# Performance work log

Measured on AMD Instinct MI355X. Metric: run time of the kernel, lower is better.

## Reference

```python
import jax, jax.numpy as jnp
import numpy as np

PATCH = 7            # args.corr_size (local correlation window)
R = PATCH // 2       # displacement radius


def _disps():
    return [(dy, dx) for dy in range(PATCH) for dx in range(PATCH)]


def setup_inputs() -> dict:
    key = jax.random.key(0)
    k1, k2, k3 = jax.random.split(key, 3)
    B, De, Do, T, H, W = 4, 64, 64, 4, 128, 128
    m_in = jax.random.normal(k1, (B, De, T, H, W), jnp.float32)
    m_out = jax.random.normal(k2, (B, Do, T, H, W), jnp.float32)
    q_in = jax.random.normal(k3, (B, De, H, W), jnp.float32)
    const = jnp.zeros((1,), jnp.float32)  # learnable constant (init 0)
    return {"m_in": m_in, "m_out": m_out, "q_in": q_in, "const": const}


def reference(m_in, m_out, q_in, const):
    B, De, T, H, W = m_in.shape
    Do = m_out.shape[1]
    P2 = PATCH * PATCH
    # --- functionCorrelation over all T frames at once ---
    # p[b, d, t, h, w] = sum_c q[b,c,h,w] * m_in[b,c,t,h+dy-R,w+dx-R]  (zero-padded)
    mp = jnp.pad(m_in, ((0, 0), (0, 0), (0, 0), (R, R), (R, R)))
    p = jnp.stack(
        [jnp.einsum('bchw,bcthw->bthw', q_in, mp[:, :, :, dy:dy + H, dx:dx + W])
         for dy, dx in _disps()],
        axis=1)  # [B, P2, T, H, W]  (matches torch stack(dim=2) then disp at dim=1)
    # --- softmax over stacked (P2*T [+1 const]) channels ---
    logits = p.reshape(B, P2 * T, H, W)
    cst = jnp.broadcast_to(const.reshape(1, 1, 1, 1), (B, 1, H, W))
    logits = jnp.concatenate([logits, cst], axis=1)
    attn = jax.nn.softmax(logits, axis=1)[:, :-1]  # drop constant channel
    attn = attn.reshape(B, P2, T, H, W)
    # --- functionCorrelationTranspose summed over T (attention read) ---
    # mem[b,c,h,w] = sum_{t,d} attn[b,d,t,h,w] * m_out[b,c,t,h+dy-R,w+dx-R]
    vp = jnp.pad(m_out, ((0, 0), (0, 0), (0, 0), (R, R), (R, R)))
    mem = jnp.zeros((B, Do, H, W), m_out.dtype)
    for d, (dy, dx) in enumerate(_disps()):
        mem = mem + jnp.einsum('bthw,bcthw->bchw', attn[:, d], vp[:, :, :, dy:dy + H, dx:dx + W])
    return mem, attn
```

## Files before the change

### kernel.cpp

```cpp
#include <hip/hip_runtime.h>

#define ATTN_OFF 4194304
#define WS_F4_COUNT 3407872ull

__global__ __launch_bounds__(256) void k1_corr(
    const float* __restrict__ m_in, const float* __restrict__ q_in,
    float* __restrict__ out)
{
  const int p = blockIdx.x + (blockIdx.y << 2) + (blockIdx.z << 6);
  const int l = ((p & 7) << 7) + (p >> 3);
  const int bx = l & 3, by = (l >> 2) & 15, bz = l >> 6;

  const int b = bz >> 2, t = bz & 3;
  const int h0 = by * 8, w0 = bx * 32;
  const int tid = threadIdx.x;
  const int tx = tid & 31, ty = tid >> 5;
  const int h = h0 + ty, w = w0 + tx;

  __shared__ float m_s[14][42][4];

  float acc[49];
#pragma unroll
  for (int d = 0; d < 49; ++d) acc[d] = 0.f;

#pragma unroll 1
  for (int cc = 0; cc < 16; ++cc) {
    __syncthreads();
    {
      const float* base = m_in + (((b * 64 + cc * 4) * 4 + t) << 14);
#pragma unroll
      for (int k = 0; k < 3; ++k) {
        const int item = tid + (k << 8);
        if (item < 532) {
          const int y  = item / 38;
          const int xi = item - 38 * y;
          const int gy = h0 - 3 + y, gx = w0 - 3 + xi;
          float4 v = make_float4(0.f, 0.f, 0.f, 0.f);
          if ((unsigned)gy < 128u && (unsigned)gx < 128u) {
            const float* p2 = base + (gy << 7) + gx;
            v.x = p2[0];
            v.y = p2[1 << 16];
            v.z = p2[2 << 16];
            v.w = p2[3 << 16];
          }
          *(float4*)&m_s[y][xi + 1][0] = v;
        }
      }
    }
    __syncthreads();

    float q0[4];
#pragma unroll
    for (int k = 0; k < 4; ++k)
      q0[k] = q_in[((b * 64 + cc * 4 + k) << 14) + (h << 7) + w];
#pragma unroll
    for (int dy = 0; dy < 7; ++dy)
#pragma unroll
      for (int dx = 0; dx < 7; ++dx) {
        const float4 mv = *(const float4*)&m_s[ty + dy][tx + 1 + dx][0];
        acc[dy * 7 + dx] += q0[0]*mv.x + q0[1]*mv.y + q0[2]*mv.z + q0[3]*mv.w;
      }
  }

  const int obase = ATTN_OFF + ((b * 196 + t) << 14) + (h << 7) + w;
#pragma unroll
  for (int d = 0; d < 49; ++d)
    out[obase + ((d * 4) << 14)] = acc[d];
}

__global__ __launch_bounds__(256) void k2_softmax(
    float* __restrict__ out, const float* __restrict__ cst,
    float4* __restrict__ ws)
{
  const int tid = threadIdx.x;
  const int pl = tid & 63;
  const int t  = tid >> 6;
  const int pix = blockIdx.x * 64 + pl;
  const int b = pix >> 14, hw = pix & 16383;
  float* base = out + ATTN_OFF + ((b * 196 + t) << 14) + hw;

  float v[49];
#pragma unroll
  for (int d = 0; d < 49; ++d) v[d] = base[(d * 4) << 14];

  float mx = -1e30f;
#pragma unroll
  for (int d = 0; d < 49; ++d) mx = fmaxf(mx, v[d]);

  __shared__ float red[4][64];
  red[t][pl] = mx;
  __syncthreads();
  float M = fmaxf(fmaxf(red[0][pl], red[1][pl]), fmaxf(red[2][pl], red[3][pl]));
  M = fmaxf(M, cst[0]);
  __syncthreads();

  float s = 0.f;
#pragma unroll
  for (int d = 0; d < 49; ++d) { v[d] = __expf(v[d] - M); s += v[d]; }
  red[t][pl] = s;
  __syncthreads();
  const float l = red[0][pl] + red[1][pl] + red[2][pl] + red[3][pl]
                + __expf(cst[0] - M);
  const float inv = 1.f / l;
#pragma unroll
  for (int d = 0; d < 49; ++d) {
    const float r = v[d] * inv;
    base[(d * 4) << 14] = r;
    v[d] = r;
  }

  if (ws) {
    const int h = hw >> 7, wc = hw & 127;
    const int G    = ((h >> 1) << 2) + (wc >> 5);
    const int lane = ((h & 1) << 5) + (wc & 31);
    float4* dst = ws + (size_t)(((b * 256 + G) * 4 + t) * 13) * 64 + lane;
#pragma unroll
    for (int g = 0; g < 13; ++g) {
      float4 p;
      p.x = v[g * 4];
      p.y = (g < 12) ? v[g * 4 + 1] : 0.f;
      p.z = (g < 12) ? v[g * 4 + 2] : 0.f;
      p.w = (g < 12) ? v[g * 4 + 3] : 0.f;
      dst[g * 64] = p;
    }
  }
}

__global__ __launch_bounds__(256) void k3_read_ws(
    const float* __restrict__ m_out, float* __restrict__ out,
    const float4* __restrict__ ws)
{
  const int b = blockIdx.z >> 3, cq = blockIdx.z & 7;
  const int h0 = blockIdx.y * 8, w0 = blockIdx.x * 32;
  const int tid = threadIdx.x;
  const int tx = tid & 31, ty = tid >> 5;
  const int h = h0 + ty, w = w0 + tx;
  const int waveid = tid >> 6, lane = tid & 63;
  const int G = ((h0 >> 1) + waveid) * 4 + blockIdx.x;

  __shared__ float m_s[2][14][42][4];

  float acc[8];
#pragma unroll
  for (int i = 0; i < 8; ++i) acc[i] = 0.f;

#pragma unroll 1
  for (int t = 0; t < 4; ++t) {
    const float4* ap = ws + (size_t)(((b * 256 + G) * 4 + t) * 13) * 64 + lane;

    __syncthreads();
    {
      const float* base = m_out + (((b * 64 + cq * 8) * 4 + t) << 14);
#pragma unroll
      for (int k = 0; k < 5; ++k) {
        const int item = tid + (k << 8);
        if (item < 1064) {
          const int quad = item >= 532;
          const int rem  = item - 532 * quad;
          const int y  = rem / 38;
          const int xi = rem - 38 * y;
          const int gy = h0 - 3 + y, gx = w0 - 3 + xi;
          float4 v = make_float4(0.f, 0.f, 0.f, 0.f);
          if ((unsigned)gy < 128u && (unsigned)gx < 128u) {
            const float* p = base + (quad << 18) + (gy << 7) + gx;
            v.x = p[0];
            v.y = p[1 << 16];
            v.z = p[2 << 16];
            v.w = p[3 << 16];
          }
          *(float4*)&m_s[quad][y][xi + 1][0] = v;
        }
      }
    }
    __syncthreads();

    float4 cur = ap[0];
#pragma unroll
    for (int g = 0; g < 13; ++g) {
      float4 nxt = cur;
      if (g < 12) nxt = ap[(g + 1) * 64];
#pragma unroll
      for (int j = 0; j < 4; ++j) {
        const int d = g * 4 + j;
        if (d >= 49) break;
        const int dy = d / 7, dx = d % 7;
        const float av = (j == 0) ? cur.x : (j == 1) ? cur.y
                       : (j == 2) ? cur.z : cur.w;
#pragma unroll
        for (int q = 0; q < 2; ++q) {
          const float4 mv = *(const float4*)&m_s[q][ty + dy][tx + dx + 1][0];
          acc[q * 4 + 0] += av * mv.x;
          acc[q * 4 + 1] += av * mv.y;
          acc[q * 4 + 2] += av * mv.z;
          acc[q * 4 + 3] += av * mv.w;
        }
      }
      cur = nxt;
    }
  }

#pragma unroll
  for (int q = 0; q < 2; ++q)
#pragma unroll
    for (int k = 0; k < 4; ++k)
      out[((b * 64 + cq * 8 + q * 4 + k) << 14) + (h << 7) + w] = acc[q * 4 + k];
}

__global__ __launch_bounds__(256) void k3_read_fb(
    const float* __restrict__ m_out, float* __restrict__ out)
{
  const int b = blockIdx.z >> 2, cq = blockIdx.z & 3;
  const int h0 = blockIdx.y * 8, w0 = blockIdx.x * 32;
  const int tid = threadIdx.x;
  const int tx = tid & 31, ty = tid >> 5;
  const int h = h0 + ty, w = w0 + tx;

  __shared__ float m_s[4][14][38][4];
  const float* __restrict__ attn = out + ATTN_OFF;

  float acc[16];
#pragma unroll
  for (int i = 0; i < 16; ++i) acc[i] = 0.f;

#pragma unroll 1
  for (int t = 0; t < 4; ++t) {
    float a[49];
#pragma unroll
    for (int d = 0; d < 49; ++d)
      a[d] = attn[((b * 196 + d * 4 + t) << 14) + (h << 7) + w];

    __syncthreads();
    for (int e = tid; e < 8512; e += 256) {
      int c16 = e / 532; int rem = e - c16 * 532;
      int y = rem / 38;  int x = rem - y * 38;
      int gy = h0 - 3 + y, gx = w0 - 3 + x;
      float v = 0.f;
      if (gy >= 0 && gy < 128 && gx >= 0 && gx < 128)
        v = m_out[(((b * 64 + cq * 16 + c16) * 4 + t) << 14) + (gy << 7) + gx];
      m_s[c16 >> 2][y][x][c16 & 3] = v;
    }
    __syncthreads();

#pragma unroll
    for (int dy = 0; dy < 7; ++dy)
#pragma unroll
      for (int dx = 0; dx < 7; ++dx) {
        const float av = a[dy * 7 + dx];
#pragma unroll
        for (int q = 0; q < 4; ++q) {
          const float4 mv = *(const float4*)&m_s[q][ty + dy][tx + dx][0];
          acc[q * 4 + 0] += av * mv.x;
          acc[q * 4 + 1] += av * mv.y;
          acc[q * 4 + 2] += av * mv.z;
          acc[q * 4 + 3] += av * mv.w;
        }
      }
  }

#pragma unroll
  for (int q = 0; q < 4; ++q)
#pragma unroll
    for (int k = 0; k < 4; ++k)
      out[((b * 64 + cq * 16 + q * 4 + k) << 14) + (h << 7) + w] = acc[q * 4 + k];
}

extern "C" void kernel_launch(void* const* d_in, const int* in_sizes, int n_in,
                              void* d_out, int out_size, void* d_ws, size_t ws_size,
                              hipStream_t stream) {
  const float* m_in  = (const float*)d_in[0];
  const float* m_out = (const float*)d_in[1];
  const float* q_in  = (const float*)d_in[2];
  const float* cst   = (const float*)d_in[3];
  float* out = (float*)d_out;

  const bool use_ws = (ws_size >= WS_F4_COUNT * 16ull) && d_ws != nullptr;
  float4* ws = use_ws ? (float4*)d_ws : nullptr;

  k1_corr<<<dim3(4, 16, 16), dim3(256), 0, stream>>>(m_in, q_in, out);
  k2_softmax<<<dim3(1024), dim3(256), 0, stream>>>(out, cst, ws);
  if (use_ws)
    k3_read_ws<<<dim3(4, 16, 32), dim3(256), 0, stream>>>(m_out, out, ws);
  else
    k3_read_fb<<<dim3(4, 16, 16), dim3(256), 0, stream>>>(m_out, out);
}
```

Baseline: 148.5 us.

## Prefetch next channel chunk into registers in correlation kernel

The correlation kernel now precomputes its halo-load offsets and boundary masks once. Inside the loop it loads the next 4-channel chunk of m_in into registers while the current chunk is being computed, so global load latency overlaps with the FMA work. Out-of-bounds pixels are handled with clamped addresses and a multiply-by-mask instead of branches. It also adds launch_bounds(256,2), which asks for two blocks per CU and may pressure registers given the 49 accumulators plus the prefetch registers.

```diff
diff --git a/kernel.cpp b/kernel.cpp
--- a/kernel.cpp
+++ b/kernel.cpp
@@ -3,7 +3,7 @@
 #define ATTN_OFF 4194304
 #define WS_F4_COUNT 3407872ull
 
-__global__ __launch_bounds__(256) void k1_corr(
+__global__ __launch_bounds__(256, 2) void k1_corr(
     const float* __restrict__ m_in, const float* __restrict__ q_in,
     float* __restrict__ out)
 {
@@ -18,36 +18,79 @@
   const int h = h0 + ty, w = w0 + tx;
 
   __shared__ float m_s[14][42][4];
+  float* const lds = &m_s[0][0][0];
 
   float acc[49];
 #pragma unroll
   for (int d = 0; d < 49; ++d) acc[d] = 0.f;
+
+  int goff0, goff1, goff2, loff0, loff1, loff2;
+  float msk0, msk1, msk2;
+  {
+    const int i0 = tid;
+    const int y0 = i0 / 38, x0 = i0 - 38 * y0;
+    const int gy0 = h0 - 3 + y0, gx0 = w0 - 3 + x0;
+    msk0 = (((unsigned)gy0 < 128u) && ((unsigned)gx0 < 128u)) ? 1.f : 0.f;
+    const int gyc0 = gy0 < 0 ? 0 : (gy0 > 127 ? 127 : gy0);
+    const int gxc0 = gx0 < 0 ? 0 : (gx0 > 127 ? 127 : gx0);
+    goff0 = (gyc0 << 7) + gxc0;
+    loff0 = (y0 * 42 + x0 + 1) << 2;
+
+    const int i1 = tid + 256;
+    const int y1 = i1 / 38, x1 = i1 - 38 * y1;
+    const int gy1 = h0 - 3 + y1, gx1 = w0 - 3 + x1;
+    msk1 = (((unsigned)gy1 < 128u) && ((unsigned)gx1 < 128u)) ? 1.f : 0.f;
+    const int gyc1 = gy1 < 0 ? 0 : (gy1 > 127 ? 127 : gy1);
+    const int gxc1 = gx1 < 0 ? 0 : (gx1 > 127 ? 127 : gx1);
+    goff1 = (gyc1 << 7) + gxc1;
+    loff1 = (y1 * 42 + x1 + 1) << 2;
+
+    const int i2 = tid + 512;
+    const int i2c = i2 < 532 ? i2 : 531;
+    const int y2 = i2c / 38, x2 = i2c - 38 * y2;
+    const int gy2 = h0 - 3 + y2, gx2 = w0 - 3 + x2;
+    msk2 = (((unsigned)gy2 < 128u) && ((unsigned)gx2 < 128u)) ? 1.f : 0.f;
+    const int gyc2 = gy2 < 0 ? 0 : (gy2 > 127 ? 127 : gy2);
+    const int gxc2 = gx2 < 0 ? 0 : (gx2 > 127 ? 127 : gx2);
+    goff2 = (gyc2 << 7) + gxc2;
+    loff2 = (y2 * 42 + x2 + 1) << 2;
+  }
+  const bool has2 = (tid < 20);
+
+  float4 r0, r1, r2;
+  {
+    const float* base = m_in + ((b * 256 + t) << 14);
+    const float* p0 = base + goff0;
+    r0.x = p0[0]; r0.y = p0[65536]; r0.z = p0[131072]; r0.w = p0[196608];
+    const float* p1 = base + goff1;
+    r1.x = p1[0]; r1.y = p1[65536]; r1.z = p1[131072]; r1.w = p1[196608];
+    r2 = make_float4(0.f, 0.f, 0.f, 0.f);
+    if (has2) {
+      const float* p2 = base + goff2;
+      r2.x = p2[0]; r2.y = p2[65536]; r2.z = p2[131072]; r2.w = p2[196608];
+    }
+  }
 
 #pragma unroll 1
   for (int cc = 0; cc < 16; ++cc) {
     __syncthreads();
-    {
-      const float* base = m_in + (((b * 64 + cc * 4) * 4 + t) << 14);
-#pragma unroll
-      for (int k = 0; k < 3; ++k) {
-        const int item = tid + (k << 8);
-        if (item < 532) {
-          const int y  = item / 38;
-          const int xi = item - 38 * y;
-          const int gy = h0 - 3 + y, gx = w0 - 3 + xi;
-          float4 v = make_float4(0.f, 0.f, 0.f, 0.f);
-          if ((unsigned)gy < 128u && (unsigned)gx < 128u) {
-            const float* p2 = base + (gy << 7) + gx;
-            v.x = p2[0];
-            v.y = p2[1 << 16];
-            v.z = p2[2 << 16];
-            v.w = p2[3 << 16];
-          }
-          *(float4*)&m_s[y][xi + 1][0] = v;
-        }
-      }
-    }
-    __syncthreads();
+    *(float4*)(lds + loff0) = make_float4(r0.x*msk0, r0.y*msk0, r0.z*msk0, r0.w*msk0);
+    *(float4*)(lds + loff1) = make_float4(r1.x*msk1, r1.y*msk1, r1.z*msk1, r1.w*msk1);
+    if (has2)
+      *(float4*)(lds + loff2) = make_float4(r2.x*msk2, r2.y*msk2, r2.z*msk2, r2.w*msk2);
+    __syncthreads();
+
+    if (cc < 15) {
+      const float* base = m_in + (((b * 64 + (cc + 1) * 4) * 4 + t) << 14);
+      const float* p0 = base + goff0;
+      r0.x = p0[0]; r0.y = p0[65536]; r0.z = p0[131072]; r0.w = p0[196608];
+      const float* p1 = base + goff1;
+      r1.x = p1[0]; r1.y = p1[65536]; r1.z = p1[131072]; r1.w = p1[196608];
+      if (has2) {
+        const float* p2 = base + goff2;
+        r2.x = p2[0]; r2.y = p2[65536]; r2.z = p2[131072]; r2.w = p2[196608];
+      }
+    }
 
     float q0[4];
 #pragma unroll
```

Measured after the change: 142.2 us. 4.2% less time.
